# Optimization experiments

Hardware: AMD Instinct MI355X
Metric: run time of the kernel (lower is better)

The kernel has to match this reference:

```python
import jax, jax.numpy as jnp
import numpy as np

N = 100000   # nodes
E = 1600000  # edges (avg degree 16)
G = 64       # graphs in the batch


def setup_inputs() -> dict:
    key = jax.random.key(0)
    ks = jax.random.split(key, 12)
    x = jax.random.normal(ks[0], (N, 1), jnp.float32)
    src = jax.random.randint(ks[1], (E,), 0, N)
    dst = jax.random.randint(ks[2], (E,), 0, N)
    batch = jnp.sort(jax.random.randint(ks[3], (N,), 0, G))
    def glorot(k, shape):
        fan_in, fan_out = shape
        lim = (6.0 / (fan_in + fan_out)) ** 0.5
        return jax.random.uniform(k, shape, jnp.float32, -lim, lim)
    return {
        "x": x, "src": src, "dst": dst, "batch": batch,
        "W1": glorot(ks[4], (1, 100)),   "b1": jnp.zeros((100,), jnp.float32),
        "W2": glorot(ks[5], (100, 200)), "b2": jnp.zeros((200,), jnp.float32),
        "Wl1": glorot(ks[6], (200, 100)), "bl1": jnp.zeros((100,), jnp.float32),
        "Wl2": glorot(ks[7], (100, 1)),   "bl2": jnp.zeros((1,), jnp.float32),
    }


def gcn_layer(x, W, b, src, dst, n_nodes):
    """PyG GCNConv: linear, then sym-normalized aggregation with self-loops, then bias."""
    h = x @ W                                   # [N, out]
    deg = jax.ops.segment_sum(jnp.ones_like(src, dtype=h.dtype), dst,
                              num_segments=n_nodes) + 1.0  # +1 for self-loop
    dinv = jax.lax.rsqrt(deg)                   # [N]
    norm = dinv[src] * dinv[dst]                # [E]
    agg = jax.ops.segment_sum(h[src] * norm[:, None], dst, num_segments=n_nodes)
    agg = agg + h * (dinv * dinv)[:, None]      # self-loop message
    return agg + b


def reference(x, src, dst, batch, W1, b1, W2, b2, Wl1, bl1, Wl2, bl2):
    n = x.shape[0]
    h = jax.nn.silu(gcn_layer(x, W1, b1, src, dst, n))       # [N,100]
    h = jax.nn.silu(gcn_layer(h, W2, b2, src, dst, n))       # [N,200]
    counts = jax.ops.segment_sum(jnp.ones((n,), h.dtype), batch, num_segments=G)
    pooled = jax.ops.segment_sum(h, batch, num_segments=G) / jnp.maximum(counts, 1.0)[:, None]
    h = jax.nn.silu(pooled @ Wl1 + bl1)                      # [G,100]
    out = h @ Wl2 + bl2                                      # [G,1]
    return out.squeeze(-1)                                   # [G]
```

## Files before the change

kernel.cpp:

```cpp
#include <hip/hip_runtime.h>
#include <math.h>

#define F1 100
#define F2 200
#define KM 16
#define BW_LOG 9
#define BW 512

__device__ __forceinline__ float siluf(float v) {
    return v / (1.0f + expf(-v));
}
__device__ __forceinline__ float silu_fast(float v) {
    return __fdividef(v, 1.0f + __expf(-v));
}

__global__ void k_batch_bounds(const int* __restrict__ batch, int N, int G,
                               int* __restrict__ starts, int* __restrict__ counts) {
    int t = threadIdx.x;
    if (t <= G) {
        int lo = 0, hi = N;
        while (lo < hi) {
            int mid = (lo + hi) >> 1;
            if (batch[mid] < t) lo = mid + 1; else hi = mid;
        }
        starts[t] = lo;
    }
    __syncthreads();
    if (t < G) counts[t] = starts[t + 1] - starts[t];
}

__global__ __launch_bounds__(256) void k_bucket_count(const int* __restrict__ dst, int E,
                                                      int nbk, int* __restrict__ gcnt) {
    extern __shared__ int cnt[];
    for (int i = threadIdx.x; i < nbk; i += 256) cnt[i] = 0;
    __syncthreads();
    for (int e = blockIdx.x * 256 + threadIdx.x; e < E; e += gridDim.x * 256)
        atomicAdd(&cnt[dst[e] >> BW_LOG], 1);
    __syncthreads();
    for (int i = threadIdx.x; i < nbk; i += 256)
        if (cnt[i]) atomicAdd(&gcnt[i], cnt[i]);
}

__global__ __launch_bounds__(256) void k_bucket_scan(const int* __restrict__ gcnt, int nbk, int E,
                                                     int* __restrict__ base, int* __restrict__ cursor) {
    __shared__ int sh[256];
    int t = threadIdx.x;
    int v = (t < nbk) ? gcnt[t] : 0;
    sh[t] = v;
    __syncthreads();
    for (int ofs = 1; ofs < 256; ofs <<= 1) {
        int u = (t >= ofs) ? sh[t - ofs] : 0;
        __syncthreads();
        sh[t] += u;
        __syncthreads();
    }
    if (t < nbk) { int ex = sh[t] - v; base[t] = ex; cursor[t] = ex; }
    if (t == 0) base[nbk] = E;
}

#define CROUND 2048
__global__ __launch_bounds__(256) void k_bucket_scatter(
    const int* __restrict__ src, const int* __restrict__ dst, int E, int nbk,
    int* __restrict__ gcursor, unsigned long long* __restrict__ pairs) {
    __shared__ int cnt[256];
    __shared__ int scanb[256];
    __shared__ int startx[256];
    __shared__ int cur[256];
    __shared__ int gbase[256];
    __shared__ unsigned long long stage[CROUND];
    int tid = threadIdx.x;
    for (long long r0 = (long long)blockIdx.x * CROUND; r0 < E; r0 += (long long)gridDim.x * CROUND) {
        cnt[tid] = 0;
        __syncthreads();
        int ss[8], dd[8], bb[8];
        bool va[8];
        #pragma unroll
        for (int j = 0; j < 8; ++j) {
            long long e = r0 + j * 256 + tid;
            va[j] = (e < E);
            if (va[j]) {
                ss[j] = src[e]; dd[j] = dst[e]; bb[j] = dd[j] >> BW_LOG;
                atomicAdd(&cnt[bb[j]], 1);
            }
        }
        __syncthreads();
        scanb[tid] = cnt[tid];
        __syncthreads();
        for (int ofs = 1; ofs < 256; ofs <<= 1) {
            int u = (tid >= ofs) ? scanb[tid - ofs] : 0;
            __syncthreads();
            scanb[tid] += u;
            __syncthreads();
        }
        int ex = scanb[tid] - cnt[tid];
        startx[tid] = ex;
        cur[tid] = ex;
        if (tid < nbk && cnt[tid] > 0) gbase[tid] = atomicAdd(&gcursor[tid], cnt[tid]);
        __syncthreads();
        int total = scanb[255];
        #pragma unroll
        for (int j = 0; j < 8; ++j) {
            if (va[j]) {
                int slot = atomicAdd(&cur[bb[j]], 1);
                stage[slot] = ((unsigned long long)(unsigned)dd[j] << 32) | (unsigned)ss[j];
            }
        }
        __syncthreads();
        for (int i = tid; i < total; i += 256) {
            unsigned long long p = stage[i];
            int b = (int)(p >> 32) >> BW_LOG;
            pairs[gbase[b] + (i - startx[b])] = p;
        }
        __syncthreads();
    }
}

__global__ __launch_bounds__(512) void k_bucket_degoff(
    const unsigned long long* __restrict__ pairs, const int* __restrict__ bbase,
    int N, float* __restrict__ dinv, int* __restrict__ off) {
    __shared__ int dl[BW];
    __shared__ int sc[BW];
    int b = blockIdx.x;
    int t = threadIdx.x;
    dl[t] = 0;
    __syncthreads();
    int beg = bbase[b], end = bbase[b + 1];
    for (int i = beg + t; i < end; i += 512)
        atomicAdd(&dl[(int)(pairs[i] >> 32) & (BW - 1)], 1);
    __syncthreads();
    int node = (b << BW_LOG) + t;
    int dg = dl[t];
    if (node < N) dinv[node] = 1.0f / sqrtf((float)dg + 1.0f);
    sc[t] = dg;
    __syncthreads();
    for (int ofs = 1; ofs < BW; ofs <<= 1) {
        int u = (t >= ofs) ? sc[t - ofs] : 0;
        __syncthreads();
        sc[t] += u;
        __syncthreads();
    }
    if (node < N) off[node] = beg + sc[t] - dg;
    if (node == N - 1) off[N] = beg + sc[t];
}

__global__ __launch_bounds__(512) void k_bucket_fill(
    const unsigned long long* __restrict__ pairs, const int* __restrict__ bbase,
    const int* __restrict__ off, const float* __restrict__ x, const float* __restrict__ dinv,
    int N, int* __restrict__ nbr, float2* __restrict__ aggxd, unsigned* __restrict__ amax) {
    __shared__ int offl[BW];
    __shared__ int cur[BW];
    __shared__ float agg[BW];
    int b = blockIdx.x;
    int t = threadIdx.x;
    int node0 = b << BW_LOG;
    int node = node0 + t;
    offl[t] = (node < N) ? off[node] : 0;
    cur[t] = 0;
    agg[t] = 0.0f;
    __syncthreads();
    int beg = bbase[b], end = bbase[b + 1];
    for (int i = beg + t; i < end; i += 512) {
        unsigned long long p = pairs[i];
        int s = (int)(p & 0xffffffffu);
        int d = (int)(p >> 32);
        int l = d & (BW - 1);
        int pos = atomicAdd(&cur[l], 1);
        nbr[offl[l] + pos] = s;
        atomicAdd(&agg[l], x[s] * dinv[s]);
    }
    __syncthreads();
    float av = 0.0f;
    if (node < N) {
        float dn = dinv[node];
        float a = dn * (agg[t] + x[node] * dn);
        aggxd[node] = make_float2(a, dn);
        av = fabsf(a);
    }
    __syncthreads();
    agg[t] = av;
    __syncthreads();
    for (int ofs = 256; ofs > 0; ofs >>= 1) {
        if (t < ofs) agg[t] = fmaxf(agg[t], agg[t + ofs]);
        __syncthreads();
    }
    if (t == 0) atomicMax(amax, __float_as_uint(agg[0]));
}

__global__ __launch_bounds__(64) void k_fit_coef(
    const float* __restrict__ W1, const float* __restrict__ b1,
    const unsigned* __restrict__ amax_bits,
    double* __restrict__ cl , float* __restrict__ scal ) {
    int j = blockIdx.x;
    int i = threadIdx.x;
    float A = __uint_as_float(*amax_bits);
    if (!(A > 0.0f)) A = 1.0f;
    A *= 1.000001f;
    if (j == 0 && i == 0) { scal[0] = A; scal[1] = 1.0f / A; }
    const double PI = 3.14159265358979323846;
    double th = (i + 0.5) * (PI / 64.0);
    double xx = cos(th);
    double w = (double)W1[j] * (double)A;
    double u = w * xx + (double)b1[j];
    double f = u / (1.0 + exp(-u));
    double acc[KM];
    {
        double c0 = 1.0, c1 = xx;
        acc[0] = f;
        acc[1] = f * xx;
        #pragma unroll
        for (int k = 2; k < KM; ++k) {
            double c2 = 2.0 * xx * c1 - c0;
            acc[k] = f * c2;
            c0 = c1; c1 = c2;
        }
    }
    #pragma unroll
    for (int k = 0; k < KM; ++k) {
        double v = acc[k];
        for (int ofs = 32; ofs > 0; ofs >>= 1)
            v += __shfl_down(v, ofs);
        if (i == 0) cl[k * F1 + j] = v * ((k == 0 ? 1.0 : 2.0) / 64.0);
    }
}

__global__ __launch_bounds__(256) void k_fit_fold(
    const double* __restrict__ cl, const float* __restrict__ W2,
    float* __restrict__ Dmat ) {
    __shared__ double scl[KM * F1];
    int tid = threadIdx.x;
    for (int idx = tid; idx < KM * F1; idx += 256) scl[idx] = cl[idx];
    __syncthreads();
    int idx = blockIdx.x * 256 + tid;
    if (idx >= KM * F2) return;
    int k = idx / F2, m = idx % F2;
    double s = 0.0;
    #pragma unroll 4
    for (int j = 0; j < F1; ++j)
        s += scl[k * F1 + j] * (double)W2[j * F2 + m];
    Dmat[idx] = (float)s;
}

__global__ __launch_bounds__(256) void k_moments(
    const int* __restrict__ off, const int* __restrict__ nbr,
    const float2* __restrict__ aggxd, const float* __restrict__ scal,
    int N, float* __restrict__ Mrow ) {
    int n = blockIdx.x * 256 + threadIdx.x;
    if (n >= N) return;
    float invA = scal[1];
    float2 sd = aggxd[n];
    float d0 = sd.y;
    float m[KM];
    {
        float xa = sd.x * invA;
        float w = d0 * d0;
        float tx = xa + xa;
        float c0 = 1.0f, c1 = xa;
        m[0] = w; m[1] = w * xa;
        #pragma unroll
        for (int k = 2; k < KM; ++k) {
            float c2 = fmaf(tx, c1, -c0);
            m[k] = w * c2;
            c0 = c1; c1 = c2;
        }
    }
    int beg = off[n], end = off[n + 1];
    for (int e = beg; e < end; ++e) {
        int s = nbr[e];
        float2 q = aggxd[s];
        float w = q.y * d0;
        float xa = q.x * invA;
        float tx = xa + xa;
        float c0 = 1.0f, c1 = xa;
        m[0] += w;
        m[1] = fmaf(w, c1, m[1]);
        #pragma unroll
        for (int k = 2; k < KM; ++k) {
            float c2 = fmaf(tx, c1, -c0);
            m[k] = fmaf(w, c2, m[k]);
            c0 = c1; c1 = c2;
        }
    }
    float4* out4 = (float4*)(Mrow + (size_t)n * KM);
    out4[0] = make_float4(m[0], m[1], m[2], m[3]);
    out4[1] = make_float4(m[4], m[5], m[6], m[7]);
    out4[2] = make_float4(m[8], m[9], m[10], m[11]);
    out4[3] = make_float4(m[12], m[13], m[14], m[15]);
}

#define P6_NODES 32
__global__ __launch_bounds__(256) void k_h2_pool6(
    const float* __restrict__ Mrow, const float* __restrict__ Dmat,
    const float* __restrict__ b2, const int* __restrict__ batch,
    int N, double* __restrict__ pooled) {
    __shared__ float sM[P6_NODES][KM];
    __shared__ int sbatch[P6_NODES];
    int tid = threadIdx.x;
    int base = blockIdx.x * P6_NODES;
    if (tid < P6_NODES * 4) {
        int node = tid >> 2, q = tid & 3;
        float4 v = make_float4(0.f, 0.f, 0.f, 0.f);
        if (base + node < N)
            v = ((const float4*)(Mrow + (size_t)(base + node) * KM))[q];
        ((float4*)&sM[node][0])[q] = v;
    }
    if (tid < P6_NODES) {
        int n = base + tid;
        sbatch[tid] = (n < N) ? batch[n] : -1;
    }
    int m = tid;
    bool act = (m < F2);
    float4 d4[KM / 4];
    float bb = 0.0f;
    if (act) {
        #pragma unroll
        for (int k = 0; k < KM / 4; ++k) {
            d4[k].x = Dmat[(4 * k + 0) * F2 + m];
            d4[k].y = Dmat[(4 * k + 1) * F2 + m];
            d4[k].z = Dmat[(4 * k + 2) * F2 + m];
            d4[k].w = Dmat[(4 * k + 3) * F2 + m];
        }
        bb = b2[m];
    }
    __syncthreads();
    double pl = 0.0;
    int gcur = -1;
    int nlim = min(P6_NODES, N - base);
    int i = 0;
    for (; i + 1 < nlim; i += 2) {
        float preA, preB;
        {
            const float4* mA = (const float4*)&sM[i][0];
            const float4* mB = (const float4*)&sM[i + 1][0];
            float4 a0 = mA[0], a1 = mA[1], a2 = mA[2], a3 = mA[3];
            float4 c0 = mB[0], c1 = mB[1], c2 = mB[2], c3 = mB[3];
            float p0 = bb, p1 = 0.f, p2 = 0.f, p3 = 0.f;
            float q0 = bb, q1 = 0.f, q2 = 0.f, q3 = 0.f;
            p0 = fmaf(a0.x, d4[0].x, p0); q0 = fmaf(c0.x, d4[0].x, q0);
            p1 = fmaf(a0.y, d4[0].y, p1); q1 = fmaf(c0.y, d4[0].y, q1);
            p2 = fmaf(a0.z, d4[0].z, p2); q2 = fmaf(c0.z, d4[0].z, q2);
            p3 = fmaf(a0.w, d4[0].w, p3); q3 = fmaf(c0.w, d4[0].w, q3);
            p0 = fmaf(a1.x, d4[1].x, p0); q0 = fmaf(c1.x, d4[1].x, q0);
            p1 = fmaf(a1.y, d4[1].y, p1); q1 = fmaf(c1.y, d4[1].y, q1);
            p2 = fmaf(a1.z, d4[1].z, p2); q2 = fmaf(c1.z, d4[1].z, q2);
            p3 = fmaf(a1.w, d4[1].w, p3); q3 = fmaf(c1.w, d4[1].w, q3);
            p0 = fmaf(a2.x, d4[2].x, p0); q0 = fmaf(c2.x, d4[2].x, q0);
            p1 = fmaf(a2.y, d4[2].y, p1); q1 = fmaf(c2.y, d4[2].y, q1);
            p2 = fmaf(a2.z, d4[2].z, p2); q2 = fmaf(c2.z, d4[2].z, q2);
            p3 = fmaf(a2.w, d4[2].w, p3); q3 = fmaf(c2.w, d4[2].w, q3);
            p0 = fmaf(a3.x, d4[3].x, p0); q0 = fmaf(c3.x, d4[3].x, q0);
            p1 = fmaf(a3.y, d4[3].y, p1); q1 = fmaf(c3.y, d4[3].y, q1);
            p2 = fmaf(a3.z, d4[3].z, p2); q2 = fmaf(c3.z, d4[3].z, q2);
            p3 = fmaf(a3.w, d4[3].w, p3); q3 = fmaf(c3.w, d4[3].w, q3);
            preA = (p0 + p1) + (p2 + p3);
            preB = (q0 + q1) + (q2 + q3);
        }
        float hA = silu_fast(preA);
        float hB = silu_fast(preB);
        int g = sbatch[i];
        if (g != gcur) {
            if (gcur >= 0 && act) atomicAdd(&pooled[(size_t)gcur * F2 + m], pl);
            pl = 0.0;
            gcur = g;
        }
        if (act) pl += (double)hA;
        g = sbatch[i + 1];
        if (g != gcur) {
            if (gcur >= 0 && act) atomicAdd(&pooled[(size_t)gcur * F2 + m], pl);
            pl = 0.0;
            gcur = g;
        }
        if (act) pl += (double)hB;
    }
    if (i < nlim) {
        const float4* m4 = (const float4*)&sM[i][0];
        float4 a0 = m4[0], a1 = m4[1], a2 = m4[2], a3 = m4[3];
        float p0 = bb, p1 = 0.f, p2 = 0.f, p3 = 0.f;
        p0 = fmaf(a0.x, d4[0].x, p0); p1 = fmaf(a0.y, d4[0].y, p1);
        p2 = fmaf(a0.z, d4[0].z, p2); p3 = fmaf(a0.w, d4[0].w, p3);
        p0 = fmaf(a1.x, d4[1].x, p0); p1 = fmaf(a1.y, d4[1].y, p1);
        p2 = fmaf(a1.z, d4[1].z, p2); p3 = fmaf(a1.w, d4[1].w, p3);
        p0 = fmaf(a2.x, d4[2].x, p0); p1 = fmaf(a2.y, d4[2].y, p1);
        p2 = fmaf(a2.z, d4[2].z, p2); p3 = fmaf(a2.w, d4[2].w, p3);
        p0 = fmaf(a3.x, d4[3].x, p0); p1 = fmaf(a3.y, d4[3].y, p1);
        p2 = fmaf(a3.z, d4[3].z, p2); p3 = fmaf(a3.w, d4[3].w, p3);
        float pre = (p0 + p1) + (p2 + p3);
        int g = sbatch[i];
        if (g != gcur) {
            if (gcur >= 0 && act) atomicAdd(&pooled[(size_t)gcur * F2 + m], pl);
            pl = 0.0;
            gcur = g;
        }
        if (act) pl += (double)silu_fast(pre);
    }
    if (gcur >= 0 && act) atomicAdd(&pooled[(size_t)gcur * F2 + m], pl);
}

#define SCHUNK 2048
__global__ __launch_bounds__(256) void k_scan_partial(const int* __restrict__ deg, int N,
                                                      int* __restrict__ partials) {
    __shared__ int red[256];
    int base = blockIdx.x * SCHUNK;
    int s = 0;
    for (int i = threadIdx.x; i < SCHUNK; i += 256) {
        int idx = base + i;
        if (idx < N) s += deg[idx];
    }
    red[threadIdx.x] = s;
    __syncthreads();
    for (int ofs = 128; ofs > 0; ofs >>= 1) {
        if (threadIdx.x < ofs) red[threadIdx.x] += red[threadIdx.x + ofs];
        __syncthreads();
    }
    if (threadIdx.x == 0) partials[blockIdx.x] = red[0];
}
__global__ __launch_bounds__(1024) void k_scan_blocks(int* __restrict__ partials, int nb) {
    __shared__ int sh[1024];
    int t = threadIdx.x;
    int v = (t < nb) ? partials[t] : 0;
    sh[t] = v;
    __syncthreads();
    for (int ofs = 1; ofs < 1024; ofs <<= 1) {
        int u = (t >= ofs) ? sh[t - ofs] : 0;
        __syncthreads();
        sh[t] += u;
        __syncthreads();
    }
    if (t < nb) partials[t] = sh[t] - v;
}
__global__ __launch_bounds__(256) void k_scan_final(const int* __restrict__ deg, int N,
                                                    const int* __restrict__ partials,
                                                    int* __restrict__ off) {
    __shared__ int sh[256];
    int base = blockIdx.x * SCHUNK;
    int i0 = base + threadIdx.x * 8;
    int v[8];
    int s = 0;
    #pragma unroll
    for (int j = 0; j < 8; ++j) {
        int idx = i0 + j;
        v[j] = (idx < N) ? deg[idx] : 0;
        s += v[j];
    }
    int mine = s;
    sh[threadIdx.x] = s;
    __syncthreads();
    for (int ofs = 1; ofs < 256; ofs <<= 1) {
        int u = (threadIdx.x >= ofs) ? sh[threadIdx.x - ofs] : 0;
        __syncthreads();
        sh[threadIdx.x] += u;
        __syncthreads();
    }
    int run = partials[blockIdx.x] + sh[threadIdx.x] - mine;
    #pragma unroll
    for (int j = 0; j < 8; ++j) {
        int idx = i0 + j;
        if (idx < N) { off[idx] = run; run += v[j]; }
    }
    if (N >= i0 && N <= i0 + 8) off[N] = run;
}
__global__ void k_count_deg(const int* __restrict__ dst, int E, int* __restrict__ deg) {
    int i = blockIdx.x * blockDim.x + threadIdx.x;
    if (i < E) atomicAdd(&deg[dst[i]], 1);
}
__global__ void k_dinv_self(const int* __restrict__ deg, const float* __restrict__ x, int N,
                            float* __restrict__ dinv, float* __restrict__ aggx) {
    int i = blockIdx.x * blockDim.x + threadIdx.x;
    if (i < N) {
        float d = 1.0f / sqrtf((float)deg[i] + 1.0f);
        dinv[i] = d;
        aggx[i] = x[i] * d * d;
    }
}
__global__ void k_fill_agg(const int* __restrict__ src, const int* __restrict__ dst, int E,
                           const int* __restrict__ off, int* __restrict__ cursor,
                           int* __restrict__ nbr,
                           const float* __restrict__ x, const float* __restrict__ dinv,
                           float* __restrict__ aggx) {
    int e = blockIdx.x * blockDim.x + threadIdx.x;
    if (e < E) {
        int s = src[e], d = dst[e];
        int p = atomicAdd(&cursor[d], 1);
        nbr[off[d] + p] = s;
        atomicAdd(&aggx[d], x[s] * dinv[s] * dinv[d]);
    }
}
__global__ __launch_bounds__(256) void k_aggh(
    const int* __restrict__ off, const int* __restrict__ nbr,
    const float* __restrict__ aggx, const float* __restrict__ dinv,
    const float* __restrict__ W1, const float* __restrict__ b1,
    int N, float* __restrict__ aggh) {
    int wave = threadIdx.x >> 6;
    int lane = threadIdx.x & 63;
    int n = blockIdx.x * 4 + wave;
    if (n >= N) return;
    int ja = lane, jb = lane + 64;
    float w1a = (ja < F1) ? W1[ja] : 0.0f;
    float b1a = (ja < F1) ? b1[ja] : 0.0f;
    float w1b = (jb < F1) ? W1[jb] : 0.0f;
    float b1b = (jb < F1) ? b1[jb] : 0.0f;
    float d0 = dinv[n];
    float a0 = aggx[n];
    float accA = silu_fast(fmaf(a0, w1a, b1a)) * (d0 * d0);
    float accB = silu_fast(fmaf(a0, w1b, b1b)) * (d0 * d0);
    int beg = off[n], end = off[n + 1];
    for (int t = beg; t < end; t += 64) {
        int cnt = min(64, end - t);
        float sa = 0.0f, sw = 0.0f;
        if (lane < cnt) {
            int s = nbr[t + lane];
            sa = aggx[s];
            sw = dinv[s] * d0;
        }
        for (int i = 0; i < cnt; ++i) {
            float ai = __shfl(sa, i);
            float wi = __shfl(sw, i);
            accA = fmaf(wi, silu_fast(fmaf(ai, w1a, b1a)), accA);
            accB = fmaf(wi, silu_fast(fmaf(ai, w1b, b1b)), accB);
        }
    }
    if (ja < F1) aggh[(size_t)n * F1 + ja] = accA;
    if (jb < F1) aggh[(size_t)n * F1 + jb] = accB;
}
#define HP_NODES 20
#define HP_KT 25
__global__ __launch_bounds__(256) void k_h2_pool3(
    const float* __restrict__ aggh, const float* __restrict__ W2, const float* __restrict__ b2,
    const int* __restrict__ batch, int N, double* __restrict__ pooled) {
    __shared__ float smem[HP_KT * F2 + HP_NODES * (F1 + 1)];
    float* sW = smem;
    float* sA = smem + HP_KT * F2;
    float* sOut = smem;
    __shared__ int sbatch[HP_NODES];
    int tid = threadIdx.x;
    int base = blockIdx.x * HP_NODES;
    for (int idx = tid; idx < HP_NODES * (F1 / 4); idx += 256) {
        int i = idx / (F1 / 4), q = idx % (F1 / 4);
        int n = base + i;
        float4 v = make_float4(0.f, 0.f, 0.f, 0.f);
        if (n < N) v = *(const float4*)(aggh + (size_t)n * F1 + q * 4);
        float* dp = &sA[i * (F1 + 1) + q * 4];
        dp[0] = v.x; dp[1] = v.y; dp[2] = v.z; dp[3] = v.w;
    }
    if (tid < HP_NODES) {
        int n = base + tid;
        sbatch[tid] = (n < N) ? batch[n] : -1;
    }
    const int fgrp = tid % 50;
    const int ngrp = tid / 50;
    const int m0 = fgrp * 4;
    const int i0 = ngrp * 4;
    const bool act = (tid < 250);
    float acc[4][4];
    #pragma unroll
    for (int i = 0; i < 4; ++i)
        #pragma unroll
        for (int j = 0; j < 4; ++j) acc[i][j] = 0.0f;
    for (int kt = 0; kt < F1; kt += HP_KT) {
        __syncthreads();
        for (int idx = tid; idx < (HP_KT * F2) / 4; idx += 256)
            ((float4*)sW)[idx] = ((const float4*)(W2 + (size_t)kt * F2))[idx];
        __syncthreads();
        if (act) {
            #pragma unroll
            for (int kk = 0; kk < HP_KT; ++kk) {
                float4 w = *(const float4*)&sW[kk * F2 + m0];
                int k = kt + kk;
                float a0 = sA[(i0 + 0) * (F1 + 1) + k];
                float a1 = sA[(i0 + 1) * (F1 + 1) + k];
                float a2 = sA[(i0 + 2) * (F1 + 1) + k];
                float a3 = sA[(i0 + 3) * (F1 + 1) + k];
                acc[0][0] = fmaf(a0, w.x, acc[0][0]); acc[0][1] = fmaf(a0, w.y, acc[0][1]);
                acc[0][2] = fmaf(a0, w.z, acc[0][2]); acc[0][3] = fmaf(a0, w.w, acc[0][3]);
                acc[1][0] = fmaf(a1, w.x, acc[1][0]); acc[1][1] = fmaf(a1, w.y, acc[1][1]);
                acc[1][2] = fmaf(a1, w.z, acc[1][2]); acc[1][3] = fmaf(a1, w.w, acc[1][3]);
                acc[2][0] = fmaf(a2, w.x, acc[2][0]); acc[2][1] = fmaf(a2, w.y, acc[2][1]);
                acc[2][2] = fmaf(a2, w.z, acc[2][2]); acc[2][3] = fmaf(a2, w.w, acc[2][3]);
                acc[3][0] = fmaf(a3, w.x, acc[3][0]); acc[3][1] = fmaf(a3, w.y, acc[3][1]);
                acc[3][2] = fmaf(a3, w.z, acc[3][2]); acc[3][3] = fmaf(a3, w.w, acc[3][3]);
            }
        }
    }
    __syncthreads();
    if (act) {
        float4 bb = *(const float4*)(b2 + m0);
        #pragma unroll
        for (int i = 0; i < 4; ++i) {
            float4 r;
            r.x = siluf(acc[i][0] + bb.x);
            r.y = siluf(acc[i][1] + bb.y);
            r.z = siluf(acc[i][2] + bb.z);
            r.w = siluf(acc[i][3] + bb.w);
            *(float4*)&sOut[(i0 + i) * F2 + m0] = r;
        }
    }
    __syncthreads();
    if (tid < F2) {
        double pl = 0.0;
        int gcur = -1;
        for (int i = 0; i < HP_NODES; ++i) {
            int n = base + i;
            if (n >= N) break;
            int g = sbatch[i];
            if (g != gcur) {
                if (gcur >= 0) atomicAdd(&pooled[(size_t)gcur * F2 + tid], pl);
                pl = 0.0;
                gcur = g;
            }
            pl += (double)sOut[i * F2 + tid];
        }
        if (gcur >= 0) atomicAdd(&pooled[(size_t)gcur * F2 + tid], pl);
    }
}

__global__ __launch_bounds__(256) void k_head(
    const double* __restrict__ pooled, const int* __restrict__ counts,
    const float* __restrict__ Wl1, const float* __restrict__ bl1,
    const float* __restrict__ Wl2, const float* __restrict__ bl2,
    float* __restrict__ out) {
    int g = blockIdx.x;
    int tid = threadIdx.x;
    __shared__ double sp[F2];
    __shared__ double red[256];
    double icnt = 1.0 / (double)max(counts[g], 1);
    for (int m = tid; m < F2; m += 256) sp[m] = pooled[(size_t)g * F2 + m] * icnt;
    __syncthreads();
    double part = 0.0;
    if (tid < 100) {
        double acc = (double)bl1[tid];
        #pragma unroll 4
        for (int m = 0; m < F2; ++m) acc += sp[m] * (double)Wl1[m * 100 + tid];
        double t1 = acc / (1.0 + exp(-acc));
        part = t1 * (double)Wl2[tid];
    }
    red[tid] = part;
    __syncthreads();
    for (int s = 128; s > 0; s >>= 1) {
        if (tid < s) red[tid] += red[tid + s];
        __syncthreads();
    }
    if (tid == 0) out[g] = (float)(red[0] + (double)bl2[0]);
}

extern "C" void kernel_launch(void* const* d_in, const int* in_sizes, int n_in,
                              void* d_out, int out_size, void* d_ws, size_t ws_size,
                              hipStream_t stream)
{
    const float* x   = (const float*)d_in[0];
    const int*   src = (const int*)d_in[1];
    const int*   dst = (const int*)d_in[2];
    const int*   batch = (const int*)d_in[3];
    const float* W1  = (const float*)d_in[4];
    const float* b1  = (const float*)d_in[5];
    const float* W2  = (const float*)d_in[6];
    const float* b2  = (const float*)d_in[7];
    const float* Wl1 = (const float*)d_in[8];
    const float* bl1 = (const float*)d_in[9];
    const float* Wl2 = (const float*)d_in[10];
    const float* bl2 = (const float*)d_in[11];
    int N = in_sizes[0];
    int E = in_sizes[1];
    int G = out_size;
    float* out = (float*)d_out;

    char* ws = (char*)d_ws;
    size_t o = 0;
    auto alloc = [&](size_t bytes) -> void* {
        o = (o + 255) & ~(size_t)255;
        void* p = ws + o;
        o += bytes;
        return p;
    };
    int nscan = (N + SCHUNK - 1) / SCHUNK;
    int nbk = (N + BW - 1) / BW;
    int*    deg    = (int*)alloc((size_t)N * 4);
    int*    cursor = (int*)alloc((size_t)N * 4);
    int*    off    = (int*)alloc((size_t)(N + 1) * 4);
    int*    nbr    = (int*)alloc((size_t)E * 4);
    float*  dinv   = (float*)alloc((size_t)N * 4);
    float*  aggx   = (float*)alloc((size_t)N * 4);
    float*  aggh   = (float*)alloc((size_t)N * F1 * 4);
    double* pooled = (double*)alloc((size_t)G * F2 * 8);
    int*    counts = (int*)alloc((size_t)G * 4);
    int*    starts = (int*)alloc((size_t)(G + 1) * 4);
    int*    partials = (int*)alloc((size_t)nscan * 4);
    int*    bcnt   = (int*)alloc((size_t)nbk * 4);
    int*    bbase  = (int*)alloc((size_t)(nbk + 1) * 4);
    int*    bcur   = (int*)alloc((size_t)nbk * 4);
    float2* aggxd  = (float2*)alloc((size_t)N * 8);
    float*  Mrow   = (float*)alloc((size_t)N * KM * 4);
    float*  Dmat   = (float*)alloc((size_t)KM * F2 * 4);
    double* clbuf  = (double*)alloc((size_t)KM * F1 * 8);
    float*  scal   = (float*)alloc(2 * 4);
    unsigned* amaxb = (unsigned*)alloc(4);
    o = (o + 255) & ~(size_t)255;
    unsigned long long* pairs = (unsigned long long*)(ws + o);
    bool use_bucket = (o + (size_t)E * 8) <= ws_size;

    hipMemsetAsync(pooled, 0, (size_t)G * F2 * 8, stream);

    int tE = (E + 255) / 256;
    int tN = (N + 255) / 256;
    k_batch_bounds<<<1, 128, 0, stream>>>(batch, N, G, starts, counts);

    if (use_bucket) {
        hipMemsetAsync(bcnt, 0, (size_t)nbk * 4, stream);
        hipMemsetAsync(amaxb, 0, 4, stream);
        k_bucket_count<<<240, 256, nbk * 4, stream>>>(dst, E, nbk, bcnt);
        k_bucket_scan<<<1, 256, 0, stream>>>(bcnt, nbk, E, bbase, bcur);
        k_bucket_scatter<<<240, 256, 0, stream>>>(src, dst, E, nbk, bcur, pairs);
        k_bucket_degoff<<<nbk, 512, 0, stream>>>(pairs, bbase, N, dinv, off);
        k_bucket_fill<<<nbk, 512, 0, stream>>>(pairs, bbase, off, x, dinv, N, nbr, aggxd, amaxb);
        k_fit_coef<<<F1, 64, 0, stream>>>(W1, b1, amaxb, clbuf, scal);
        k_fit_fold<<<(KM * F2 + 255) / 256, 256, 0, stream>>>(clbuf, W2, Dmat);
        k_moments<<<(N + 255) / 256, 256, 0, stream>>>(off, nbr, aggxd, scal, N, Mrow);
        k_h2_pool6<<<(N + P6_NODES - 1) / P6_NODES, 256, 0, stream>>>(Mrow, Dmat, b2, batch, N, pooled);
    } else {
        hipMemsetAsync(deg, 0, (size_t)N * 4, stream);
        hipMemsetAsync(cursor, 0, (size_t)N * 4, stream);
        k_count_deg<<<tE, 256, 0, stream>>>(dst, E, deg);
        k_dinv_self<<<tN, 256, 0, stream>>>(deg, x, N, dinv, aggx);
        k_scan_partial<<<nscan, 256, 0, stream>>>(deg, N, partials);
        k_scan_blocks<<<1, 1024, 0, stream>>>(partials, nscan);
        k_scan_final<<<nscan, 256, 0, stream>>>(deg, N, partials, off);
        k_fill_agg<<<tE, 256, 0, stream>>>(src, dst, E, off, cursor, nbr, x, dinv, aggx);
        k_aggh<<<(N + 3) / 4, 256, 0, stream>>>(off, nbr, aggx, dinv, W1, b1, N, aggh);
        k_h2_pool3<<<(N + HP_NODES - 1) / HP_NODES, 256, 0, stream>>>(aggh, W2, b2, batch, N, pooled);
    }
    k_head<<<G, 256, 0, stream>>>(pooled, counts, Wl1, bl1, Wl2, bl2, out);
}
```

Baseline: 171.7 us.

## Replace CSR build with bucketed shared-memory atomic moment accumulation

Removes the per-node CSR construction (offset scan and nbr fill) and instead accumulates the 16 Chebyshev moments per destination directly from the dst-bucketed edge pairs, using shared-memory atomics with padded rows of 17. It also precomputes x*dinv into a separate array so the aggregation kernel reads one value per edge. This avoids writing and re-reading the neighbour list and the scan work. In exchange it adds 16 shared atomics per edge and 34KB of LDS per block, which may reduce occupancy and cause atomic contention on high-degree nodes.

```diff
diff --git a/kernel.cpp b/kernel.cpp
--- a/kernel.cpp
+++ b/kernel.cpp
@@ -6,6 +6,7 @@
 #define KM 16
 #define BW_LOG 9
 #define BW 512
+#define MP 17
 
 __device__ __forceinline__ float siluf(float v) {
     return v / (1.0f + expf(-v));
@@ -115,11 +116,11 @@
     }
 }
 
-__global__ __launch_bounds__(512) void k_bucket_degoff(
+__global__ __launch_bounds__(512) void k_bucket_deg2(
     const unsigned long long* __restrict__ pairs, const int* __restrict__ bbase,
-    int N, float* __restrict__ dinv, int* __restrict__ off) {
+    const float* __restrict__ x, int N,
+    float* __restrict__ dinv, float* __restrict__ y) {
     __shared__ int dl[BW];
-    __shared__ int sc[BW];
     int b = blockIdx.x;
     int t = threadIdx.x;
     dl[t] = 0;
@@ -129,50 +130,35 @@
         atomicAdd(&dl[(int)(pairs[i] >> 32) & (BW - 1)], 1);
     __syncthreads();
     int node = (b << BW_LOG) + t;
-    int dg = dl[t];
-    if (node < N) dinv[node] = 1.0f / sqrtf((float)dg + 1.0f);
-    sc[t] = dg;
-    __syncthreads();
-    for (int ofs = 1; ofs < BW; ofs <<= 1) {
-        int u = (t >= ofs) ? sc[t - ofs] : 0;
-        __syncthreads();
-        sc[t] += u;
-        __syncthreads();
-    }
-    if (node < N) off[node] = beg + sc[t] - dg;
-    if (node == N - 1) off[N] = beg + sc[t];
-}
-
-__global__ __launch_bounds__(512) void k_bucket_fill(
+    if (node < N) {
+        float d = 1.0f / sqrtf((float)dl[t] + 1.0f);
+        dinv[node] = d;
+        y[node] = x[node] * d;
+    }
+}
+
+__global__ __launch_bounds__(512) void k_bucket_aggx(
     const unsigned long long* __restrict__ pairs, const int* __restrict__ bbase,
-    const int* __restrict__ off, const float* __restrict__ x, const float* __restrict__ dinv,
-    int N, int* __restrict__ nbr, float2* __restrict__ aggxd, unsigned* __restrict__ amax) {
-    __shared__ int offl[BW];
-    __shared__ int cur[BW];
+    const float* __restrict__ y, const float* __restrict__ dinv, int N,
+    float2* __restrict__ aggxd, unsigned* __restrict__ amax) {
     __shared__ float agg[BW];
     int b = blockIdx.x;
     int t = threadIdx.x;
-    int node0 = b << BW_LOG;
-    int node = node0 + t;
-    offl[t] = (node < N) ? off[node] : 0;
-    cur[t] = 0;
     agg[t] = 0.0f;
     __syncthreads();
     int beg = bbase[b], end = bbase[b + 1];
     for (int i = beg + t; i < end; i += 512) {
         unsigned long long p = pairs[i];
         int s = (int)(p & 0xffffffffu);
-        int d = (int)(p >> 32);
-        int l = d & (BW - 1);
-        int pos = atomicAdd(&cur[l], 1);
-        nbr[offl[l] + pos] = s;
-        atomicAdd(&agg[l], x[s] * dinv[s]);
+        int l = (int)(p >> 32) & (BW - 1);
+        atomicAdd(&agg[l], y[s]);
     }
     __syncthreads();
     float av = 0.0f;
+    int node = (b << BW_LOG) + t;
     if (node < N) {
         float dn = dinv[node];
-        float a = dn * (agg[t] + x[node] * dn);
+        float a = dn * (agg[t] + y[node]);
         aggxd[node] = make_float2(a, dn);
         av = fabsf(a);
     }
@@ -240,51 +226,60 @@
     Dmat[idx] = (float)s;
 }
 
-__global__ __launch_bounds__(256) void k_moments(
-    const int* __restrict__ off, const int* __restrict__ nbr,
-    const float2* __restrict__ aggxd, const float* __restrict__ scal,
-    int N, float* __restrict__ Mrow ) {
-    int n = blockIdx.x * 256 + threadIdx.x;
-    if (n >= N) return;
+__global__ __launch_bounds__(512) void k_bucket_moments(
+    const unsigned long long* __restrict__ pairs, const int* __restrict__ bbase,
+    const float2* __restrict__ aggxd, const float* __restrict__ scal, int N,
+    float* __restrict__ Mrow ) {
+    __shared__ float ml[BW * MP];
+    int b = blockIdx.x;
+    int t = threadIdx.x;
+    for (int i = t; i < BW * MP; i += 512) ml[i] = 0.0f;
+    __syncthreads();
     float invA = scal[1];
-    float2 sd = aggxd[n];
-    float d0 = sd.y;
-    float m[KM];
-    {
-        float xa = sd.x * invA;
-        float w = d0 * d0;
+    int beg = bbase[b], end = bbase[b + 1];
+    for (int i = beg + t; i < end; i += 512) {
+        unsigned long long p = pairs[i];
+        int s = (int)(p & 0xffffffffu);
+        int l = (int)(p >> 32) & (BW - 1);
+        float2 q = aggxd[s];
+        float w = q.y;
+        float xa = q.x * invA;
         float tx = xa + xa;
+        float* mb = &ml[l * MP];
         float c0 = 1.0f, c1 = xa;
-        m[0] = w; m[1] = w * xa;
+        atomicAdd(&mb[0], w);
+        atomicAdd(&mb[1], w * xa);
         #pragma unroll
         for (int k = 2; k < KM; ++k) {
             float c2 = fmaf(tx, c1, -c0);
-            m[k] = w * c2;
+            atomicAdd(&mb[k], w * c2);
             c0 = c1; c1 = c2;
         }
     }
-    int beg = off[n], end = off[n + 1];
-    for (int e = beg; e < end; ++e) {
-        int s = nbr[e];
-        float2 q = aggxd[s];
-        float w = q.y * d0;
-        float xa = q.x * invA;
+    __syncthreads();
+    int node = (b << BW_LOG) + t;
+    if (node < N) {
+        float2 sd = aggxd[node];
+        float d0 = sd.y;
+        float xa = sd.x * invA;
         float tx = xa + xa;
+        const float* mb = &ml[t * MP];
+        float m[KM];
         float c0 = 1.0f, c1 = xa;
-        m[0] += w;
-        m[1] = fmaf(w, c1, m[1]);
+        m[0] = d0 * (mb[0] + d0);
+        m[1] = d0 * (mb[1] + d0 * xa);
         #pragma unroll
         for (int k = 2; k < KM; ++k) {
             float c2 = fmaf(tx, c1, -c0);
-            m[k] = fmaf(w, c2, m[k]);
+            m[k] = d0 * (mb[k] + d0 * c2);
             c0 = c1; c1 = c2;
         }
-    }
-    float4* out4 = (float4*)(Mrow + (size_t)n * KM);
-    out4[0] = make_float4(m[0], m[1], m[2], m[3]);
-    out4[1] = make_float4(m[4], m[5], m[6], m[7]);
-    out4[2] = make_float4(m[8], m[9], m[10], m[11]);
-    out4[3] = make_float4(m[12], m[13], m[14], m[15]);
+        float4* out4 = (float4*)(Mrow + (size_t)node * KM);
+        out4[0] = make_float4(m[0], m[1], m[2], m[3]);
+        out4[1] = make_float4(m[4], m[5], m[6], m[7]);
+        out4[2] = make_float4(m[8], m[9], m[10], m[11]);
+        out4[3] = make_float4(m[12], m[13], m[14], m[15]);
+    }
 }
 
 #define P6_NODES 32
@@ -678,6 +673,7 @@
     int*    nbr    = (int*)alloc((size_t)E * 4);
     float*  dinv   = (float*)alloc((size_t)N * 4);
     float*  aggx   = (float*)alloc((size_t)N * 4);
+    float*  yv     = (float*)alloc((size_t)N * 4);
     float*  aggh   = (float*)alloc((size_t)N * F1 * 4);
     double* pooled = (double*)alloc((size_t)G * F2 * 8);
     int*    counts = (int*)alloc((size_t)G * 4);
@@ -708,11 +704,11 @@
         k_bucket_count<<<240, 256, nbk * 4, stream>>>(dst, E, nbk, bcnt);
         k_bucket_scan<<<1, 256, 0, stream>>>(bcnt, nbk, E, bbase, bcur);
         k_bucket_scatter<<<240, 256, 0, stream>>>(src, dst, E, nbk, bcur, pairs);
-        k_bucket_degoff<<<nbk, 512, 0, stream>>>(pairs, bbase, N, dinv, off);
-        k_bucket_fill<<<nbk, 512, 0, stream>>>(pairs, bbase, off, x, dinv, N, nbr, aggxd, amaxb);
+        k_bucket_deg2<<<nbk, 512, 0, stream>>>(pairs, bbase, x, N, dinv, yv);
+        k_bucket_aggx<<<nbk, 512, 0, stream>>>(pairs, bbase, yv, dinv, N, aggxd, amaxb);
         k_fit_coef<<<F1, 64, 0, stream>>>(W1, b1, amaxb, clbuf, scal);
         k_fit_fold<<<(KM * F2 + 255) / 256, 256, 0, stream>>>(clbuf, W2, Dmat);
-        k_moments<<<(N + 255) / 256, 256, 0, stream>>>(off, nbr, aggxd, scal, N, Mrow);
+        k_bucket_moments<<<nbk, 512, 0, stream>>>(pairs, bbase, aggxd, scal, N, Mrow);
         k_h2_pool6<<<(N + P6_NODES - 1) / P6_NODES, 256, 0, stream>>>(Mrow, Dmat, b2, batch, N, pooled);
     } else {
         hipMemsetAsync(deg, 0, (size_t)N * 4, stream);
```

After: 316.8 us. 84.5% more time.
